# Optimization experiments

Hardware: AMD Instinct MI355X
Metric: run time of the kernel (lower is better)

The kernel has to match this reference:

```python
import jax, jax.numpy as jnp
import numpy as np

B, S, D, H = 2, 2048, 1024, 16
HD = D // H

def setup_inputs() -> dict:
    key = jax.random.key(0)
    ks = jax.random.split(key, 9)
    s = 1.0 / np.sqrt(D)
    return {
        "x": jax.random.normal(ks[0], (B, S, D), dtype=jnp.float32),
        "Wq": jax.random.uniform(ks[1], (D, D), jnp.float32, -s, s),
        "bq": jax.random.uniform(ks[2], (D,), jnp.float32, -s, s),
        "Wk": jax.random.uniform(ks[3], (D, D), jnp.float32, -s, s),
        "bk": jax.random.uniform(ks[4], (D,), jnp.float32, -s, s),
        "Wv": jax.random.uniform(ks[5], (D, D), jnp.float32, -s, s),
        "bv": jax.random.uniform(ks[6], (D,), jnp.float32, -s, s),
        "Wo": jax.random.uniform(ks[7], (D, D), jnp.float32, -s, s),
        "bo": jax.random.uniform(ks[8], (D,), jnp.float32, -s, s),
    }

def reference(x, Wq, bq, Wk, bk, Wv, bv, Wo, bo):
    # project and split heads: [B,S,D] -> [B,H,S,HD]
    def heads(t):
        return t.reshape(B, S, H, HD).transpose(0, 2, 1, 3)
    q = heads(x @ Wq.T + bq)
    k = heads(x @ Wk.T + bk)
    v = heads(x @ Wv.T + bv)
    scores = jnp.einsum('bhqd,bhkd->bhqk', q, k) / np.sqrt(HD).astype(np.float32)
    attention_weights = jax.nn.softmax(scores, axis=-1)  # [B,H,S,S]
    out = jnp.einsum('bhqk,bhkd->bhqd', attention_weights, v)
    out = out.transpose(0, 2, 1, 3).reshape(B, S, D)
    out = out @ Wo.T + bo
    return out, attention_weights
```

## Files before the change

kernel.cpp:

```cpp
#include <hip/hip_runtime.h>
#include <stdint.h>

#define BB 2
#define SS 2048
#define DD 1024
#define HH 16
#define HDD 64

typedef _Float16 f16x8 __attribute__((ext_vector_type(8)));
typedef _Float16 f16x4 __attribute__((ext_vector_type(4)));
typedef float f32x4 __attribute__((ext_vector_type(4)));

#define MFMA16(a,b,c) __builtin_amdgcn_mfma_f32_16x16x32_f16((a),(b),(c),0,0,0)

__device__ __forceinline__ _Float16 toh(float v) { return (_Float16)v; }

__device__ __forceinline__ void gll16(const void* g, void* l) {
  __builtin_amdgcn_global_load_lds(
      (const __attribute__((address_space(1))) unsigned int*)g,
      (__attribute__((address_space(3))) unsigned int*)l, 16, 0, 0);
}

__global__ __launch_bounds__(256) void k_convert(
    const float* __restrict__ x, const float* __restrict__ Wq, const float* __restrict__ Wk,
    const float* __restrict__ Wv, const float* __restrict__ Wo, _Float16* __restrict__ ws) {
  int i = blockIdx.x * 256 + threadIdx.x;
  const float4* src; _Float16* dst; int idx;
  if (i < 1048576) { src = (const float4*)x; dst = ws; idx = i; }
  else {
    int j = i - 1048576;
    int wsel = j >> 18;
    idx = j & 262143;
    src = (const float4*)(wsel == 0 ? Wq : wsel == 1 ? Wk : wsel == 2 ? Wv : Wo);
    dst = ws + 4194304 + (size_t)wsel * 1048576;
  }
  float4 f = src[idx];
  f16x4 o = { toh(f.x), toh(f.y), toh(f.z), toh(f.w) };
  *(f16x4*)(dst + (size_t)idx * 4) = o;
}

__device__ __forceinline__ void stage2(const _Float16* g, _Float16* lds, int t) {
#pragma unroll
  for (int i = 0; i < 2; ++i) {
    const _Float16* src = g + (size_t)(i * 64 + (t >> 2)) * 1024 + (t & 3) * 8;
    gll16(src, lds + i * 2048 + t * 8);
  }
}

__device__ __forceinline__ void gemm_core(const _Float16* __restrict__ A,
                                          const _Float16* __restrict__ W,
                                          int bm, int bn, _Float16* As, _Float16* Bs,
                                          f32x4 (&acc)[4][4]) {
  const int t = threadIdx.x;
  const int l = t & 63, w = t >> 6;
  const int wr = w >> 1, wc = w & 1, li = l & 15, lg = l >> 4;
  const _Float16* Abase = A + (size_t)bm * 128 * 1024;
  const _Float16* Wbase = W + (size_t)bn * 128 * 1024;

  stage2(Abase, As, t);
  stage2(Wbase, Bs, t);
  int cur = 0;
  for (int kt = 0; kt < 32; ++kt) {
    __syncthreads();
    if (kt < 31) {
      stage2(Abase + (kt + 1) * 32, As + (cur ^ 1) * 4096, t);
      stage2(Wbase + (kt + 1) * 32, Bs + (cur ^ 1) * 4096, t);
    }
    const _Float16* Ab = As + cur * 4096;
    const _Float16* Bb = Bs + cur * 4096;
    f16x8 af[4], bfr[4];
#pragma unroll
    for (int m = 0; m < 4; ++m)
      af[m] = *(const f16x8*)(Ab + (wr * 64 + m * 16 + li) * 32 + lg * 8);
#pragma unroll
    for (int n = 0; n < 4; ++n)
      bfr[n] = *(const f16x8*)(Bb + (wc * 64 + n * 16 + li) * 32 + lg * 8);
    __builtin_amdgcn_s_setprio(1);
#pragma unroll
    for (int m = 0; m < 4; ++m)
#pragma unroll
      for (int n = 0; n < 4; ++n)
        acc[m][n] = MFMA16(af[m], bfr[n], acc[m][n]);
    __builtin_amdgcn_s_setprio(0);
    cur ^= 1;
  }
}

__global__ __launch_bounds__(256) void k_gemm_qkv(
    const _Float16* __restrict__ xb, const _Float16* __restrict__ wqb,
    const _Float16* __restrict__ wkb, const _Float16* __restrict__ wvb,
    const float* __restrict__ bq, const float* __restrict__ bk, const float* __restrict__ bv,
    _Float16* __restrict__ Qw, _Float16* __restrict__ Kw, _Float16* __restrict__ Vtw) {
  int mode = blockIdx.z;
  const _Float16* W = mode == 0 ? wqb : mode == 1 ? wkb : wvb;
  const float* bias = mode == 0 ? bq : mode == 1 ? bk : bv;
  __shared__ _Float16 As[8192], Bs[8192];
  f32x4 acc[4][4] = {};
  gemm_core(xb, W, blockIdx.y, blockIdx.x, As, Bs, acc);

  int t = threadIdx.x, l = t & 63, w = t >> 6, wr = w >> 1, wc = w & 1, li = l & 15, lg = l >> 4;
  int rb = blockIdx.y * 128 + wr * 64, cb = blockIdx.x * 128 + wc * 64;
  float scale = (mode == 0) ? 0.125f : 1.0f;
#pragma unroll
  for (int n = 0; n < 4; ++n) {
    int col = cb + n * 16 + li;
    float bsv = bias[col];
    int hh = col >> 6, hd = col & 63;
#pragma unroll
    for (int m = 0; m < 4; ++m)
#pragma unroll
      for (int r = 0; r < 4; ++r) {
        int row = rb + m * 16 + lg * 4 + r;
        int bb = row >> 11, ssi = row & 2047;
        float val = (acc[m][n][r] + bsv) * scale;
        if (mode == 0)
          Qw[((size_t)(bb * HH + hh) * SS + ssi) * HDD + hd] = toh(val);
        else if (mode == 1)
          Kw[((size_t)(bb * HH + hh) * SS + ssi) * HDD + hd] = toh(val);
        else
          Vtw[((size_t)(bb * HH + hh) * HDD + hd) * SS + ssi] = toh(val);
      }
  }
}

__global__ __launch_bounds__(256) void k_flash(
    const _Float16* __restrict__ Qw, const _Float16* __restrict__ Kw,
    const _Float16* __restrict__ Vtw, float* __restrict__ mlb, _Float16* __restrict__ attnb) {
  int qb = blockIdx.x;
  int h = blockIdx.y, b = blockIdx.z;
  int t = threadIdx.x, l = t & 63, w = t >> 6;
  int li = l & 15, lg = l >> 4;
  size_t bh = (size_t)(b * HH + h);
  const _Float16* Qh = Qw + bh * SS * HDD;
  const _Float16* Kh = Kw + bh * SS * HDD;
  const _Float16* Vh = Vtw + bh * HDD * SS;
  int qrow = qb * 64 + w * 16;

  __shared__ _Float16 Kbuf[2][4096];
  __shared__ _Float16 Vbuf[2][4096];
  __shared__ _Float16 Wl[4][16][72];

  f16x8 aq0 = *(const f16x8*)&Qh[(size_t)(qrow + li) * HDD + lg * 8];
  f16x8 aq1 = *(const f16x8*)&Qh[(size_t)(qrow + li) * HDD + 32 + lg * 8];

  const f32x4 fzero = {0.f, 0.f, 0.f, 0.f};
  f32x4 oacc[4] = {fzero, fzero, fzero, fzero};
  float lsum[4] = {0.f, 0.f, 0.f, 0.f};

  auto STAGE = [&](int kt, int sel) {
    int kb = kt * 64;
#pragma unroll
    for (int c2 = 0; c2 < 2; ++c2) {
      int s = c2 * 256 + t;
      int row = s >> 3, cc = (s & 7) ^ (row & 7);
      gll16(Kh + (size_t)(kb + row) * HDD + cc * 8, (void*)&Kbuf[sel][s * 8]);
      gll16(Vh + (size_t)row * SS + kb + cc * 8, (void*)&Vbuf[sel][s * 8]);
    }
  };

  STAGE(0, 0);
  __syncthreads();
  int cur = 0;
  for (int kt = 0; kt < 32; ++kt) {
    if (kt < 31) STAGE(kt + 1, cur ^ 1);
    const _Float16* Kb = Kbuf[cur];
    f32x4 sf[4];
    __builtin_amdgcn_s_setprio(1);
#pragma unroll
    for (int f = 0; f < 4; ++f) {
      int row = f * 16 + li;
      f16x8 k0 = *(const f16x8*)(Kb + row * 64 + ((lg ^ (row & 7)) * 8));
      f16x8 k1 = *(const f16x8*)(Kb + row * 64 + (((lg + 4) ^ (row & 7)) * 8));
      f32x4 a = MFMA16(aq0, k0, fzero);
      sf[f] = MFMA16(aq1, k1, a);
    }
    __builtin_amdgcn_s_setprio(0);
#pragma unroll
    for (int f = 0; f < 4; ++f)
#pragma unroll
      for (int r = 0; r < 4; ++r) {
        float p = __expf(sf[f][r]);
        lsum[r] += p;
        Wl[w][lg * 4 + r][f * 16 + li] = toh(p);
      }
    f16x8 aw0 = *(const f16x8*)&Wl[w][li][lg * 8];
    f16x8 aw1 = *(const f16x8*)&Wl[w][li][32 + lg * 8];
    const _Float16* Vb = Vbuf[cur];
    __builtin_amdgcn_s_setprio(1);
#pragma unroll
    for (int n = 0; n < 4; ++n) {
      int row = n * 16 + li;
      f16x8 v0 = *(const f16x8*)(Vb + row * 64 + ((lg ^ (row & 7)) * 8));
      f16x8 v1 = *(const f16x8*)(Vb + row * 64 + (((lg + 4) ^ (row & 7)) * 8));
      oacc[n] = MFMA16(aw0, v0, oacc[n]);
      oacc[n] = MFMA16(aw1, v1, oacc[n]);
    }
    __builtin_amdgcn_s_setprio(0);
    __syncthreads();
    cur ^= 1;
  }

#pragma unroll
  for (int d = 1; d < 16; d <<= 1)
#pragma unroll
    for (int r = 0; r < 4; ++r) lsum[r] += __shfl_xor(lsum[r], d);
  float rinv[4];
#pragma unroll
  for (int r = 0; r < 4; ++r) rinv[r] = 1.0f / lsum[r];

#pragma unroll
  for (int n = 0; n < 4; ++n)
#pragma unroll
    for (int r = 0; r < 4; ++r) {
      int q = qrow + lg * 4 + r;
      attnb[((size_t)b * SS + q) * DD + h * 64 + n * 16 + li] = toh(oacc[n][r] * rinv[r]);
    }
  if (li == 0) {
#pragma unroll
    for (int r = 0; r < 4; ++r) {
      int q = qrow + lg * 4 + r;
      mlb[bh * SS + q] = rinv[r];
    }
  }
}

__global__ __launch_bounds__(256) void k_wts(
    const _Float16* __restrict__ Qw, const _Float16* __restrict__ Kw,
    const float* __restrict__ mlb, float* __restrict__ wts) {
  int ktile = blockIdx.x, qtile = blockIdx.y;
  size_t bh = blockIdx.z;
  const _Float16* Qh = Qw + bh * SS * HDD;
  const _Float16* Kh = Kw + bh * SS * HDD;
  __shared__ _Float16 As[8192], Bs[8192];
  int t = threadIdx.x, l = t & 63, w = t >> 6, wr = w >> 1, wc = w & 1, li = l & 15, lg = l >> 4;

#pragma unroll
  for (int c4 = 0; c4 < 4; ++c4) {
    int s = c4 * 256 + t;
    int row = s >> 3, cc = (s & 7) ^ (row & 7);
    gll16(Qh + (size_t)(qtile * 128 + row) * HDD + cc * 8, (void*)&As[s * 8]);
    gll16(Kh + (size_t)(ktile * 128 + row) * HDD + cc * 8, (void*)&Bs[s * 8]);
  }
  __syncthreads();

  f32x4 acc[4][4] = {};
#pragma unroll
  for (int s = 0; s < 2; ++s) {
    f16x8 af[4], bf[4];
#pragma unroll
    for (int m = 0; m < 4; ++m) {
      int row = wr * 64 + m * 16 + li;
      af[m] = *(const f16x8*)(As + row * 64 + (((s * 4 + lg) ^ (row & 7)) * 8));
    }
#pragma unroll
    for (int n = 0; n < 4; ++n) {
      int row = wc * 64 + n * 16 + li;
      bf[n] = *(const f16x8*)(Bs + row * 64 + (((s * 4 + lg) ^ (row & 7)) * 8));
    }
    __builtin_amdgcn_s_setprio(1);
#pragma unroll
    for (int m = 0; m < 4; ++m)
#pragma unroll
      for (int n = 0; n < 4; ++n)
        acc[m][n] = MFMA16(af[m], bf[n], acc[m][n]);
    __builtin_amdgcn_s_setprio(0);
  }

  int rb = qtile * 128 + wr * 64, cb = ktile * 128 + wc * 64;
#pragma unroll
  for (int m = 0; m < 4; ++m)
#pragma unroll
    for (int r = 0; r < 4; ++r) {
      int qr = rb + m * 16 + lg * 4 + r;
      float ri = mlb[bh * SS + qr];
      float* wb = wts + ((bh * SS + qr) * (size_t)SS) + cb;
#pragma unroll
      for (int n = 0; n < 4; ++n)
        wb[n * 16 + li] = __expf(acc[m][n][r]) * ri;
    }
}

__global__ __launch_bounds__(256) void k_gemm_o(
    const _Float16* __restrict__ attnb, const _Float16* __restrict__ wob,
    const float* __restrict__ bo, float* __restrict__ outp) {
  __shared__ _Float16 As[8192], Bs[8192];
  f32x4 acc[4][4] = {};
  gemm_core(attnb, wob, blockIdx.y, blockIdx.x, As, Bs, acc);

  int t = threadIdx.x, l = t & 63, w = t >> 6, wr = w >> 1, wc = w & 1, li = l & 15, lg = l >> 4;
  int rb = blockIdx.y * 128 + wr * 64, cb = blockIdx.x * 128 + wc * 64;
#pragma unroll
  for (int n = 0; n < 4; ++n) {
    int col = cb + n * 16 + li;
    float bsv = bo[col];
#pragma unroll
    for (int m = 0; m < 4; ++m)
#pragma unroll
      for (int r = 0; r < 4; ++r) {
        int row = rb + m * 16 + lg * 4 + r;
        outp[(size_t)row * DD + col] = acc[m][n][r] + bsv;
      }
  }
}

extern "C" void kernel_launch(void* const* d_in, const int* in_sizes, int n_in,
                              void* d_out, int out_size, void* d_ws, size_t ws_size,
                              hipStream_t stream) {
  const float* x  = (const float*)d_in[0];
  const float* Wq = (const float*)d_in[1];
  const float* bq = (const float*)d_in[2];
  const float* Wk = (const float*)d_in[3];
  const float* bk = (const float*)d_in[4];
  const float* Wv = (const float*)d_in[5];
  const float* bv = (const float*)d_in[6];
  const float* Wo = (const float*)d_in[7];
  const float* bo = (const float*)d_in[8];

  _Float16* ws   = (_Float16*)d_ws;
  _Float16* xb   = ws;
  _Float16* wqb  = ws + 4194304;
  _Float16* wkb  = ws + 5242880;
  _Float16* wvb  = ws + 6291456;
  _Float16* wob  = ws + 7340032;
  _Float16* Qw   = ws + 8388608;
  _Float16* Kw   = ws + 12582912;
  _Float16* Vtw  = ws + 16777216;
  _Float16* attnb= ws + 20971520;
  float* mlb = (float*)(ws + 4194304);

  float* outp = (float*)d_out;
  float* wts  = outp + 4194304;

  k_convert<<<dim3(8192), dim3(256), 0, stream>>>(x, Wq, Wk, Wv, Wo, ws);
  k_gemm_qkv<<<dim3(8, 32, 3), dim3(256), 0, stream>>>(xb, wqb, wkb, wvb, bq, bk, bv, Qw, Kw, Vtw);
  k_flash<<<dim3(32, 16, 2), dim3(256), 0, stream>>>(Qw, Kw, Vtw, mlb, attnb);
  k_wts<<<dim3(16, 16, 32), dim3(256), 0, stream>>>(Qw, Kw, mlb, wts);
  k_gemm_o<<<dim3(8, 32, 1), dim3(256), 0, stream>>>(attnb, wob, bo, outp);
}
```

Before: 277.9 us.

## Split softmax into row-sum pass and fused weights-write plus PV pass

Result: slower. 296.9 us (+6.8%).

```diff
diff --git a/kernel.cpp b/kernel.cpp
--- a/kernel.cpp
+++ b/kernel.cpp
@@ -123,9 +123,9 @@
   }
 }
 
-__global__ __launch_bounds__(256) void k_flash(
+__global__ __launch_bounds__(256) void k_sums(
     const _Float16* __restrict__ Qw, const _Float16* __restrict__ Kw,
-    const _Float16* __restrict__ Vtw, float* __restrict__ mlb, _Float16* __restrict__ attnb) {
+    float* __restrict__ mlb) {
   int qb = blockIdx.x;
   int h = blockIdx.y, b = blockIdx.z;
   int t = threadIdx.x, l = t & 63, w = t >> 6;
@@ -133,18 +133,14 @@
   size_t bh = (size_t)(b * HH + h);
   const _Float16* Qh = Qw + bh * SS * HDD;
   const _Float16* Kh = Kw + bh * SS * HDD;
-  const _Float16* Vh = Vtw + bh * HDD * SS;
   int qrow = qb * 64 + w * 16;
 
   __shared__ _Float16 Kbuf[2][4096];
-  __shared__ _Float16 Vbuf[2][4096];
-  __shared__ _Float16 Wl[4][16][72];
 
   f16x8 aq0 = *(const f16x8*)&Qh[(size_t)(qrow + li) * HDD + lg * 8];
   f16x8 aq1 = *(const f16x8*)&Qh[(size_t)(qrow + li) * HDD + 32 + lg * 8];
 
   const f32x4 fzero = {0.f, 0.f, 0.f, 0.f};
-  f32x4 oacc[4] = {fzero, fzero, fzero, fzero};
   float lsum[4] = {0.f, 0.f, 0.f, 0.f};
 
   auto STAGE = [&](int kt, int sel) {
@@ -154,7 +150,6 @@
       int s = c2 * 256 + t;
       int row = s >> 3, cc = (s & 7) ^ (row & 7);
       gll16(Kh + (size_t)(kb + row) * HDD + cc * 8, (void*)&Kbuf[sel][s * 8]);
-      gll16(Vh + (size_t)row * SS + kb + cc * 8, (void*)&Vbuf[sel][s * 8]);
     }
   };
 
@@ -178,13 +173,108 @@
 #pragma unroll
     for (int f = 0; f < 4; ++f)
 #pragma unroll
-      for (int r = 0; r < 4; ++r) {
-        float p = __expf(sf[f][r]);
-        lsum[r] += p;
-        Wl[w][lg * 4 + r][f * 16 + li] = toh(p);
-      }
-    f16x8 aw0 = *(const f16x8*)&Wl[w][li][lg * 8];
-    f16x8 aw1 = *(const f16x8*)&Wl[w][li][32 + lg * 8];
+      for (int r = 0; r < 4; ++r)
+        lsum[r] += __expf(sf[f][r]);
+    __syncthreads();
+    cur ^= 1;
+  }
+
+#pragma unroll
+  for (int d = 1; d < 16; d <<= 1)
+#pragma unroll
+    for (int r = 0; r < 4; ++r) lsum[r] += __shfl_xor(lsum[r], d);
+  if (li == 0) {
+#pragma unroll
+    for (int r = 0; r < 4; ++r)
+      mlb[bh * SS + qrow + lg * 4 + r] = 1.0f / lsum[r];
+  }
+}
+
+__global__ __launch_bounds__(256) void k_wts_pv(
+    const _Float16* __restrict__ Qw, const _Float16* __restrict__ Kw,
+    const _Float16* __restrict__ Vtw, const float* __restrict__ mlb,
+    float* __restrict__ wts, _Float16* __restrict__ attnb) {
+  int qtile = blockIdx.x;
+  int bhi = blockIdx.y;
+  int b = bhi >> 4, h = bhi & 15;
+  int t = threadIdx.x, l = t & 63, w = t >> 6;
+  int li = l & 15, lg = l >> 4;
+  size_t bh = (size_t)bhi;
+  const _Float16* Qh = Qw + bh * SS * HDD;
+  const _Float16* Kh = Kw + bh * SS * HDD;
+  const _Float16* Vh = Vtw + bh * HDD * SS;
+  int qrow = qtile * 128 + w * 32;
+
+  __shared__ _Float16 Kbuf[2][4096];
+  __shared__ _Float16 Vbuf[2][4096];
+  __shared__ _Float16 Wl[4][32][72];
+
+  f16x8 aq[2][2];
+#pragma unroll
+  for (int qh = 0; qh < 2; ++qh)
+#pragma unroll
+    for (int s = 0; s < 2; ++s)
+      aq[qh][s] = *(const f16x8*)&Qh[(size_t)(qrow + qh * 16 + li) * HDD + s * 32 + lg * 8];
+
+  float rinv[2][4];
+#pragma unroll
+  for (int qh = 0; qh < 2; ++qh)
+#pragma unroll
+    for (int r = 0; r < 4; ++r)
+      rinv[qh][r] = mlb[bh * SS + qrow + qh * 16 + lg * 4 + r];
+
+  const f32x4 fzero = {0.f, 0.f, 0.f, 0.f};
+  f32x4 oacc[2][4] = {{fzero, fzero, fzero, fzero}, {fzero, fzero, fzero, fzero}};
+
+  auto STAGE = [&](int kt, int sel) {
+    int kb = kt * 64;
+#pragma unroll
+    for (int c2 = 0; c2 < 2; ++c2) {
+      int s = c2 * 256 + t;
+      int row = s >> 3, cc = (s & 7) ^ (row & 7);
+      gll16(Kh + (size_t)(kb + row) * HDD + cc * 8, (void*)&Kbuf[sel][s * 8]);
+      gll16(Vh + (size_t)row * SS + kb + cc * 8, (void*)&Vbuf[sel][s * 8]);
+    }
+  };
+
+  STAGE(0, 0);
+  __syncthreads();
+  int cur = 0;
+  for (int kt = 0; kt < 32; ++kt) {
+    int kb = kt * 64;
+    if (kt < 31) STAGE(kt + 1, cur ^ 1);
+    const _Float16* Kb = Kbuf[cur];
+    f32x4 sf[4][2];
+    __builtin_amdgcn_s_setprio(1);
+#pragma unroll
+    for (int f = 0; f < 4; ++f) {
+      int row = f * 16 + li;
+      f16x8 k0 = *(const f16x8*)(Kb + row * 64 + ((lg ^ (row & 7)) * 8));
+      f16x8 k1 = *(const f16x8*)(Kb + row * 64 + (((lg + 4) ^ (row & 7)) * 8));
+#pragma unroll
+      for (int qh = 0; qh < 2; ++qh) {
+        f32x4 a = MFMA16(aq[qh][0], k0, fzero);
+        sf[f][qh] = MFMA16(aq[qh][1], k1, a);
+      }
+    }
+    __builtin_amdgcn_s_setprio(0);
+#pragma unroll
+    for (int f = 0; f < 4; ++f)
+#pragma unroll
+      for (int qh = 0; qh < 2; ++qh)
+#pragma unroll
+        for (int r = 0; r < 4; ++r) {
+          float wv = __expf(sf[f][qh][r]) * rinv[qh][r];
+          int qr = qrow + qh * 16 + lg * 4 + r;
+          wts[((bh * SS + qr) * (size_t)SS) + kb + f * 16 + li] = wv;
+          Wl[w][qh * 16 + lg * 4 + r][f * 16 + li] = toh(wv);
+        }
+    f16x8 pa[2][2];
+#pragma unroll
+    for (int qh = 0; qh < 2; ++qh)
+#pragma unroll
+      for (int ks = 0; ks < 2; ++ks)
+        pa[qh][ks] = *(const f16x8*)&Wl[w][qh * 16 + li][ks * 32 + lg * 8];
     const _Float16* Vb = Vbuf[cur];
     __builtin_amdgcn_s_setprio(1);
 #pragma unroll
@@ -192,8 +282,11 @@
       int row = n * 16 + li;
       f16x8 v0 = *(const f16x8*)(Vb + row * 64 + ((lg ^ (row & 7)) * 8));
       f16x8 v1 = *(const f16x8*)(Vb + row * 64 + (((lg + 4) ^ (row & 7)) * 8));
-      oacc[n] = MFMA16(aw0, v0, oacc[n]);
-      oacc[n] = MFMA16(aw1, v1, oacc[n]);
+#pragma unroll
+      for (int qh = 0; qh < 2; ++qh) {
+        oacc[qh][n] = MFMA16(pa[qh][0], v0, oacc[qh][n]);
+        oacc[qh][n] = MFMA16(pa[qh][1], v1, oacc[qh][n]);
+      }
     }
     __builtin_amdgcn_s_setprio(0);
     __syncthreads();
@@ -201,83 +294,14 @@
   }
 
 #pragma unroll
-  for (int d = 1; d < 16; d <<= 1)
-#pragma unroll
-    for (int r = 0; r < 4; ++r) lsum[r] += __shfl_xor(lsum[r], d);
-  float rinv[4];
-#pragma unroll
-  for (int r = 0; r < 4; ++r) rinv[r] = 1.0f / lsum[r];
-
-#pragma unroll
-  for (int n = 0; n < 4; ++n)
-#pragma unroll
-    for (int r = 0; r < 4; ++r) {
-      int q = qrow + lg * 4 + r;
-      attnb[((size_t)b * SS + q) * DD + h * 64 + n * 16 + li] = toh(oacc[n][r] * rinv[r]);
-    }
-  if (li == 0) {
-#pragma unroll
-    for (int r = 0; r < 4; ++r) {
-      int q = qrow + lg * 4 + r;
-      mlb[bh * SS + q] = rinv[r];
-    }
-  }
-}
-
-__global__ __launch_bounds__(256) void k_wts(
-    const _Float16* __restrict__ Qw, const _Float16* __restrict__ Kw,
-    const float* __restrict__ mlb, float* __restrict__ wts) {
-  int ktile = blockIdx.x, qtile = blockIdx.y;
-  size_t bh = blockIdx.z;
-  const _Float16* Qh = Qw + bh * SS * HDD;
-  const _Float16* Kh = Kw + bh * SS * HDD;
-  __shared__ _Float16 As[8192], Bs[8192];
-  int t = threadIdx.x, l = t & 63, w = t >> 6, wr = w >> 1, wc = w & 1, li = l & 15, lg = l >> 4;
-
-#pragma unroll
-  for (int c4 = 0; c4 < 4; ++c4) {
-    int s = c4 * 256 + t;
-    int row = s >> 3, cc = (s & 7) ^ (row & 7);
-    gll16(Qh + (size_t)(qtile * 128 + row) * HDD + cc * 8, (void*)&As[s * 8]);
-    gll16(Kh + (size_t)(ktile * 128 + row) * HDD + cc * 8, (void*)&Bs[s * 8]);
-  }
-  __syncthreads();
-
-  f32x4 acc[4][4] = {};
-#pragma unroll
-  for (int s = 0; s < 2; ++s) {
-    f16x8 af[4], bf[4];
-#pragma unroll
-    for (int m = 0; m < 4; ++m) {
-      int row = wr * 64 + m * 16 + li;
-      af[m] = *(const f16x8*)(As + row * 64 + (((s * 4 + lg) ^ (row & 7)) * 8));
-    }
-#pragma unroll
-    for (int n = 0; n < 4; ++n) {
-      int row = wc * 64 + n * 16 + li;
-      bf[n] = *(const f16x8*)(Bs + row * 64 + (((s * 4 + lg) ^ (row & 7)) * 8));
-    }
-    __builtin_amdgcn_s_setprio(1);
-#pragma unroll
-    for (int m = 0; m < 4; ++m)
-#pragma unroll
-      for (int n = 0; n < 4; ++n)
-        acc[m][n] = MFMA16(af[m], bf[n], acc[m][n]);
-    __builtin_amdgcn_s_setprio(0);
-  }
-
-  int rb = qtile * 128 + wr * 64, cb = ktile * 128 + wc * 64;
-#pragma unroll
-  for (int m = 0; m < 4; ++m)
-#pragma unroll
-    for (int r = 0; r < 4; ++r) {
-      int qr = rb + m * 16 + lg * 4 + r;
-      float ri = mlb[bh * SS + qr];
-      float* wb = wts + ((bh * SS + qr) * (size_t)SS) + cb;
-#pragma unroll
-      for (int n = 0; n < 4; ++n)
-        wb[n * 16 + li] = __expf(acc[m][n][r]) * ri;
-    }
+  for (int qh = 0; qh < 2; ++qh)
+#pragma unroll
+    for (int n = 0; n < 4; ++n)
+#pragma unroll
+      for (int r = 0; r < 4; ++r) {
+        int q = qrow + qh * 16 + lg * 4 + r;
+        attnb[((size_t)b * SS + q) * DD + h * 64 + n * 16 + li] = toh(oacc[qh][n][r]);
+      }
 }
 
 __global__ __launch_bounds__(256) void k_gemm_o(
@@ -333,7 +357,7 @@
 
   k_convert<<<dim3(8192), dim3(256), 0, stream>>>(x, Wq, Wk, Wv, Wo, ws);
   k_gemm_qkv<<<dim3(8, 32, 3), dim3(256), 0, stream>>>(xb, wqb, wkb, wvb, bq, bk, bv, Qw, Kw, Vtw);
-  k_flash<<<dim3(32, 16, 2), dim3(256), 0, stream>>>(Qw, Kw, Vtw, mlb, attnb);
-  k_wts<<<dim3(16, 16, 32), dim3(256), 0, stream>>>(Qw, Kw, mlb, wts);
+  k_sums<<<dim3(32, 16, 2), dim3(256), 0, stream>>>(Qw, Kw, mlb);
+  k_wts_pv<<<dim3(16, 32), dim3(256), 0, stream>>>(Qw, Kw, Vtw, mlb, wts, attnb);
   k_gemm_o<<<dim3(8, 32, 1), dim3(256), 0, stream>>>(attnb, wob, bo, outp);
 }
```

## Load K/V directly from global in flash kernel and fold log2e into Q scale

Applied to the files above, without the earlier changes.

New measurement: 429.7 us. +54.6%, slower.

```diff
diff --git a/kernel.cpp b/kernel.cpp
--- a/kernel.cpp
+++ b/kernel.cpp
@@ -100,7 +100,7 @@
 
   int t = threadIdx.x, l = t & 63, w = t >> 6, wr = w >> 1, wc = w & 1, li = l & 15, lg = l >> 4;
   int rb = blockIdx.y * 128 + wr * 64, cb = blockIdx.x * 128 + wc * 64;
-  float scale = (mode == 0) ? 0.125f : 1.0f;
+  float scale = (mode == 0) ? 0.125f * 1.4426950408889634f : 1.0f;
 #pragma unroll
   for (int n = 0; n < 4; ++n) {
     int col = cb + n * 16 + li;
@@ -136,8 +136,6 @@
   const _Float16* Vh = Vtw + bh * HDD * SS;
   int qrow = qb * 64 + w * 16;
 
-  __shared__ _Float16 Kbuf[2][4096];
-  __shared__ _Float16 Vbuf[2][4096];
   __shared__ _Float16 Wl[4][16][72];
 
   f16x8 aq0 = *(const f16x8*)&Qh[(size_t)(qrow + li) * HDD + lg * 8];
@@ -147,30 +145,15 @@
   f32x4 oacc[4] = {fzero, fzero, fzero, fzero};
   float lsum[4] = {0.f, 0.f, 0.f, 0.f};
 
-  auto STAGE = [&](int kt, int sel) {
+  for (int kt = 0; kt < 32; ++kt) {
     int kb = kt * 64;
-#pragma unroll
-    for (int c2 = 0; c2 < 2; ++c2) {
-      int s = c2 * 256 + t;
-      int row = s >> 3, cc = (s & 7) ^ (row & 7);
-      gll16(Kh + (size_t)(kb + row) * HDD + cc * 8, (void*)&Kbuf[sel][s * 8]);
-      gll16(Vh + (size_t)row * SS + kb + cc * 8, (void*)&Vbuf[sel][s * 8]);
-    }
-  };
-
-  STAGE(0, 0);
-  __syncthreads();
-  int cur = 0;
-  for (int kt = 0; kt < 32; ++kt) {
-    if (kt < 31) STAGE(kt + 1, cur ^ 1);
-    const _Float16* Kb = Kbuf[cur];
     f32x4 sf[4];
     __builtin_amdgcn_s_setprio(1);
 #pragma unroll
     for (int f = 0; f < 4; ++f) {
-      int row = f * 16 + li;
-      f16x8 k0 = *(const f16x8*)(Kb + row * 64 + ((lg ^ (row & 7)) * 8));
-      f16x8 k1 = *(const f16x8*)(Kb + row * 64 + (((lg + 4) ^ (row & 7)) * 8));
+      const _Float16* kp = &Kh[(size_t)(kb + f * 16 + li) * HDD + lg * 8];
+      f16x8 k0 = *(const f16x8*)kp;
+      f16x8 k1 = *(const f16x8*)(kp + 32);
       f32x4 a = MFMA16(aq0, k0, fzero);
       sf[f] = MFMA16(aq1, k1, a);
     }
@@ -179,25 +162,22 @@
     for (int f = 0; f < 4; ++f)
 #pragma unroll
       for (int r = 0; r < 4; ++r) {
-        float p = __expf(sf[f][r]);
+        float p = exp2f(sf[f][r]);
         lsum[r] += p;
         Wl[w][lg * 4 + r][f * 16 + li] = toh(p);
       }
     f16x8 aw0 = *(const f16x8*)&Wl[w][li][lg * 8];
     f16x8 aw1 = *(const f16x8*)&Wl[w][li][32 + lg * 8];
-    const _Float16* Vb = Vbuf[cur];
     __builtin_amdgcn_s_setprio(1);
 #pragma unroll
     for (int n = 0; n < 4; ++n) {
-      int row = n * 16 + li;
-      f16x8 v0 = *(const f16x8*)(Vb + row * 64 + ((lg ^ (row & 7)) * 8));
-      f16x8 v1 = *(const f16x8*)(Vb + row * 64 + (((lg + 4) ^ (row & 7)) * 8));
+      const _Float16* vp = &Vh[(size_t)(n * 16 + li) * SS + kb + lg * 8];
+      f16x8 v0 = *(const f16x8*)vp;
+      f16x8 v1 = *(const f16x8*)(vp + 32);
       oacc[n] = MFMA16(aw0, v0, oacc[n]);
       oacc[n] = MFMA16(aw1, v1, oacc[n]);
     }
     __builtin_amdgcn_s_setprio(0);
-    __syncthreads();
-    cur ^= 1;
   }
 
 #pragma unroll
@@ -276,7 +256,7 @@
       float* wb = wts + ((bh * SS + qr) * (size_t)SS) + cb;
 #pragma unroll
       for (int n = 0; n < 4; ++n)
-        wb[n * 16 + li] = __expf(acc[m][n][r]) * ri;
+        wb[n * 16 + li] = exp2f(acc[m][n][r]) * ri;
     }
 }
 
```

## Process 32 query rows per wave in flash kernel and use exp2 with folded log2e

Applied to the files above, without the earlier changes.

Measured after the change: 275.3 us. No clear change (-0.9%).

```diff
diff --git a/kernel.cpp b/kernel.cpp
--- a/kernel.cpp
+++ b/kernel.cpp
@@ -100,7 +100,7 @@
 
   int t = threadIdx.x, l = t & 63, w = t >> 6, wr = w >> 1, wc = w & 1, li = l & 15, lg = l >> 4;
   int rb = blockIdx.y * 128 + wr * 64, cb = blockIdx.x * 128 + wc * 64;
-  float scale = (mode == 0) ? 0.125f : 1.0f;
+  float scale = (mode == 0) ? 0.125f * 1.4426950408889634f : 1.0f;
 #pragma unroll
   for (int n = 0; n < 4; ++n) {
     int col = cb + n * 16 + li;
@@ -134,18 +134,22 @@
   const _Float16* Qh = Qw + bh * SS * HDD;
   const _Float16* Kh = Kw + bh * SS * HDD;
   const _Float16* Vh = Vtw + bh * HDD * SS;
-  int qrow = qb * 64 + w * 16;
+  int qrow = qb * 128 + w * 32;
 
   __shared__ _Float16 Kbuf[2][4096];
   __shared__ _Float16 Vbuf[2][4096];
-  __shared__ _Float16 Wl[4][16][72];
-
-  f16x8 aq0 = *(const f16x8*)&Qh[(size_t)(qrow + li) * HDD + lg * 8];
-  f16x8 aq1 = *(const f16x8*)&Qh[(size_t)(qrow + li) * HDD + 32 + lg * 8];
+  __shared__ _Float16 Wl[4][32][72];
+
+  f16x8 aq[2][2];
+#pragma unroll
+  for (int qh = 0; qh < 2; ++qh)
+#pragma unroll
+    for (int s = 0; s < 2; ++s)
+      aq[qh][s] = *(const f16x8*)&Qh[(size_t)(qrow + qh * 16 + li) * HDD + s * 32 + lg * 8];
 
   const f32x4 fzero = {0.f, 0.f, 0.f, 0.f};
-  f32x4 oacc[4] = {fzero, fzero, fzero, fzero};
-  float lsum[4] = {0.f, 0.f, 0.f, 0.f};
+  f32x4 oacc[2][4] = {{fzero, fzero, fzero, fzero}, {fzero, fzero, fzero, fzero}};
+  float lsum[2][4] = {{0.f, 0.f, 0.f, 0.f}, {0.f, 0.f, 0.f, 0.f}};
 
   auto STAGE = [&](int kt, int sel) {
     int kb = kt * 64;
@@ -164,27 +168,36 @@
   for (int kt = 0; kt < 32; ++kt) {
     if (kt < 31) STAGE(kt + 1, cur ^ 1);
     const _Float16* Kb = Kbuf[cur];
-    f32x4 sf[4];
+    f32x4 sf[4][2];
     __builtin_amdgcn_s_setprio(1);
 #pragma unroll
     for (int f = 0; f < 4; ++f) {
       int row = f * 16 + li;
       f16x8 k0 = *(const f16x8*)(Kb + row * 64 + ((lg ^ (row & 7)) * 8));
       f16x8 k1 = *(const f16x8*)(Kb + row * 64 + (((lg + 4) ^ (row & 7)) * 8));
-      f32x4 a = MFMA16(aq0, k0, fzero);
-      sf[f] = MFMA16(aq1, k1, a);
+#pragma unroll
+      for (int qh = 0; qh < 2; ++qh) {
+        f32x4 a = MFMA16(aq[qh][0], k0, fzero);
+        sf[f][qh] = MFMA16(aq[qh][1], k1, a);
+      }
     }
     __builtin_amdgcn_s_setprio(0);
 #pragma unroll
     for (int f = 0; f < 4; ++f)
 #pragma unroll
-      for (int r = 0; r < 4; ++r) {
-        float p = __expf(sf[f][r]);
-        lsum[r] += p;
-        Wl[w][lg * 4 + r][f * 16 + li] = toh(p);
-      }
-    f16x8 aw0 = *(const f16x8*)&Wl[w][li][lg * 8];
-    f16x8 aw1 = *(const f16x8*)&Wl[w][li][32 + lg * 8];
+      for (int qh = 0; qh < 2; ++qh)
+#pragma unroll
+        for (int r = 0; r < 4; ++r) {
+          float p = exp2f(sf[f][qh][r]);
+          lsum[qh][r] += p;
+          Wl[w][qh * 16 + lg * 4 + r][f * 16 + li] = toh(p);
+        }
+    f16x8 pa[2][2];
+#pragma unroll
+    for (int qh = 0; qh < 2; ++qh)
+#pragma unroll
+      for (int ks = 0; ks < 2; ++ks)
+        pa[qh][ks] = *(const f16x8*)&Wl[w][qh * 16 + li][ks * 32 + lg * 8];
     const _Float16* Vb = Vbuf[cur];
     __builtin_amdgcn_s_setprio(1);
 #pragma unroll
@@ -192,8 +205,11 @@
       int row = n * 16 + li;
       f16x8 v0 = *(const f16x8*)(Vb + row * 64 + ((lg ^ (row & 7)) * 8));
       f16x8 v1 = *(const f16x8*)(Vb + row * 64 + (((lg + 4) ^ (row & 7)) * 8));
-      oacc[n] = MFMA16(aw0, v0, oacc[n]);
-      oacc[n] = MFMA16(aw1, v1, oacc[n]);
+#pragma unroll
+      for (int qh = 0; qh < 2; ++qh) {
+        oacc[qh][n] = MFMA16(pa[qh][0], v0, oacc[qh][n]);
+        oacc[qh][n] = MFMA16(pa[qh][1], v1, oacc[qh][n]);
+      }
     }
     __builtin_amdgcn_s_setprio(0);
     __syncthreads();
@@ -203,24 +219,33 @@
 #pragma unroll
   for (int d = 1; d < 16; d <<= 1)
 #pragma unroll
-    for (int r = 0; r < 4; ++r) lsum[r] += __shfl_xor(lsum[r], d);
-  float rinv[4];
-#pragma unroll
-  for (int r = 0; r < 4; ++r) rinv[r] = 1.0f / lsum[r];
-
-#pragma unroll
-  for (int n = 0; n < 4; ++n)
-#pragma unroll
-    for (int r = 0; r < 4; ++r) {
-      int q = qrow + lg * 4 + r;
-      attnb[((size_t)b * SS + q) * DD + h * 64 + n * 16 + li] = toh(oacc[n][r] * rinv[r]);
-    }
+    for (int qh = 0; qh < 2; ++qh)
+#pragma unroll
+      for (int r = 0; r < 4; ++r) lsum[qh][r] += __shfl_xor(lsum[qh][r], d);
+  float rinv[2][4];
+#pragma unroll
+  for (int qh = 0; qh < 2; ++qh)
+#pragma unroll
+    for (int r = 0; r < 4; ++r) rinv[qh][r] = 1.0f / lsum[qh][r];
+
+#pragma unroll
+  for (int qh = 0; qh < 2; ++qh)
+#pragma unroll
+    for (int n = 0; n < 4; ++n)
+#pragma unroll
+      for (int r = 0; r < 4; ++r) {
+        int q = qrow + qh * 16 + lg * 4 + r;
+        attnb[((size_t)b * SS + q) * DD + h * 64 + n * 16 + li] =
+            toh(oacc[qh][n][r] * rinv[qh][r]);
+      }
   if (li == 0) {
 #pragma unroll
-    for (int r = 0; r < 4; ++r) {
-      int q = qrow + lg * 4 + r;
-      mlb[bh * SS + q] = rinv[r];
-    }
+    for (int qh = 0; qh < 2; ++qh)
+#pragma unroll
+      for (int r = 0; r < 4; ++r) {
+        int q = qrow + qh * 16 + lg * 4 + r;
+        mlb[bh * SS + q] = rinv[qh][r];
+      }
   }
 }
 
@@ -276,7 +301,7 @@
       float* wb = wts + ((bh * SS + qr) * (size_t)SS) + cb;
 #pragma unroll
       for (int n = 0; n < 4; ++n)
-        wb[n * 16 + li] = __expf(acc[m][n][r]) * ri;
+        wb[n * 16 + li] = exp2f(acc[m][n][r]) * ri;
     }
 }
 
@@ -333,7 +358,7 @@
 
   k_convert<<<dim3(8192), dim3(256), 0, stream>>>(x, Wq, Wk, Wv, Wo, ws);
   k_gemm_qkv<<<dim3(8, 32, 3), dim3(256), 0, stream>>>(xb, wqb, wkb, wvb, bq, bk, bv, Qw, Kw, Vtw);
-  k_flash<<<dim3(32, 16, 2), dim3(256), 0, stream>>>(Qw, Kw, Vtw, mlb, attnb);
+  k_flash<<<dim3(16, 16, 2), dim3(256), 0, stream>>>(Qw, Kw, Vtw, mlb, attnb);
   k_wts<<<dim3(16, 16, 32), dim3(256), 0, stream>>>(Qw, Kw, mlb, wts);
   k_gemm_o<<<dim3(8, 32, 1), dim3(256), 0, stream>>>(attnb, wob, bo, outp);
 }
```
